# Kernel optimization log

Measured on AMD Instinct MI355X. Metric: run time of the kernel, lower is better.

## Reference

```python
import jax, jax.numpy as jnp
import numpy as np
from math import sqrt

B, N, D = 8, 4096, 512

def rotary(x, phases):
    # x: [B,N,D], phases: [B,N,D/2]
    c, s = jnp.cos(phases), jnp.sin(phases)
    a, b = jnp.split(x, 2, axis=-1)
    return jnp.concatenate([a * c - b * s, a * s + b * c], axis=-1)

def setup_inputs() -> dict:
    key = jax.random.key(0)
    ks = jax.random.split(key, 8)
    phi = jax.random.normal(ks[0], (B, N, D), dtype=jnp.float32)
    coords = jax.random.normal(ks[1], (B, N, 3), dtype=jnp.float32)
    weights = jax.random.uniform(ks[2], (B, N), dtype=jnp.float32)
    std = 1.0 / sqrt(D)
    Wq = jax.random.normal(ks[3], (D, D), dtype=jnp.float32) * std
    Wk = jax.random.normal(ks[4], (D, D), dtype=jnp.float32) * std
    Wv = jax.random.normal(ks[5], (D, D), dtype=jnp.float32) * std
    bq = jnp.zeros((D,), jnp.float32)
    bk = jnp.zeros((D,), jnp.float32)
    bv = jnp.zeros((D,), jnp.float32)
    # mode_lift weight, std = 1/kernel_scale with kernel_scale=1.0
    Wrot = jax.random.normal(ks[6], (D // 2, 3), dtype=jnp.float32)
    return {"phi": phi, "coords": coords, "weights": weights,
            "Wq": Wq, "bq": bq, "Wk": Wk, "bk": bk, "Wv": Wv, "bv": bv,
            "Wrot": Wrot}

def reference(phi, coords, weights, Wq, bq, Wk, bk, Wv, bv, Wrot):
    d = phi.shape[-1]
    q = phi @ Wq.T + bq
    k = phi @ Wk.T + bk
    v = phi @ Wv.T + bv
    # _normalize: scale query by 1/sqrt(d); attach quadrature weights to value
    q = q * (1.0 / sqrt(d))
    v = weights[..., None] * v
    # rotary positional encoding on q and k
    phases = jnp.einsum('bnc,dc->bnd', coords, Wrot)  # [B,N,D/2]
    q = rotary(q, phases)
    k = rotary(k, phases)
    # linear attention: q @ (k^T @ v), O(N*d^2)
    kv = jnp.einsum('bnd,bne->bde', k, v)   # [B,D,D]
    return jnp.einsum('bnd,bde->bne', q, kv)  # [B,N,D]
```

## Files before the change

kernel.cpp:

```cpp
#include <hip/hip_runtime.h>


typedef _Float16 f16x8 __attribute__((ext_vector_type(8)));
typedef _Float16 f16x4 __attribute__((ext_vector_type(4)));
typedef float f32x4 __attribute__((ext_vector_type(4)));

__device__ __forceinline__ void gl_lds16(const void* g, void* l) {
    __builtin_amdgcn_global_load_lds(
        (const __attribute__((address_space(1))) void*)g,
        (__attribute__((address_space(3))) void*)l, 16, 0, 0);
}

__device__ __forceinline__ void stage2(const _Float16* gA, size_t sA,
                                       const _Float16* gB, size_t sB,
                                       _Float16* As, _Float16* Bs,
                                       int ca, int srow, int sseg) {
    gl_lds16(&gA[(size_t)(ca * 16 + srow) * sA + sseg], &As[ca * 512]);
    gl_lds16(&gA[(size_t)(ca * 16 + 16 + srow) * sA + sseg], &As[(ca + 1) * 512]);
    gl_lds16(&gB[(size_t)(ca * 16 + srow) * sB + sseg], &Bs[ca * 512]);
    gl_lds16(&gB[(size_t)(ca * 16 + 16 + srow) * sB + sseg], &Bs[(ca + 1) * 512]);
}

__device__ __forceinline__ void mfma_step(const _Float16* As, const _Float16* Bs,
                                          int wm, int wn, int l16, int qs,
                                          f32x4 acc[4][4]) {
    f16x8 af[4], bf[4];
    #pragma unroll
    for (int mi = 0; mi < 4; mi++)
        af[mi] = *(const f16x8*)&As[(wm + mi * 16 + l16) * 32 + qs * 8];
    #pragma unroll
    for (int ni = 0; ni < 4; ni++)
        bf[ni] = *(const f16x8*)&Bs[(wn + ni * 16 + l16) * 32 + qs * 8];
    #pragma unroll
    for (int mi = 0; mi < 4; mi++)
        #pragma unroll
        for (int ni = 0; ni < 4; ni++)
            acc[mi][ni] = __builtin_amdgcn_mfma_f32_16x16x32_f16(
                af[mi], bf[ni], acc[mi][ni], 0, 0, 0);
}

#define PIPE_LOOP3(gA, sA, gB, sB)                                            \
    stage2(gA, sA, gB, sB, Asr[0], Bsr[0], ca, srow, sseg);                   \
    stage2(gA + 32, sA, gB + 32, sB, Asr[1], Bsr[1], ca, srow, sseg);         \
    _Pragma("unroll")                                                         \
    for (int t = 0; t < 16; t++) {                                            \
        asm volatile("s_waitcnt lgkmcnt(0)" ::: "memory");                    \
        __builtin_amdgcn_sched_barrier(0);                                    \
        if (t < 15) { asm volatile("s_waitcnt vmcnt(4)" ::: "memory"); }      \
        else        { asm volatile("s_waitcnt vmcnt(0)" ::: "memory"); }      \
        __builtin_amdgcn_s_barrier();                                         \
        asm volatile("" ::: "memory");                                        \
        __builtin_amdgcn_sched_barrier(0);                                    \
        if (t + 2 < 16)                                                       \
            stage2(gA + (size_t)(t + 2) * 32, sA,                             \
                   gB + (size_t)(t + 2) * 32, sB,                             \
                   Asr[(t + 2) % 3], Bsr[(t + 2) % 3], ca, srow, sseg);       \
        __builtin_amdgcn_s_setprio(1);                                        \
        mfma_step(Asr[t % 3], Bsr[t % 3], wm, wn, l16, qs, acc);              \
        __builtin_amdgcn_s_setprio(0);                                        \
    }

#define RING_PTRS(smem)                                                       \
    _Float16* Asr[3] = {(_Float16*)(smem), (_Float16*)(smem + 16384),         \
                        (_Float16*)(smem + 32768)};                           \
    _Float16* Bsr[3] = {(_Float16*)(smem + 8192), (_Float16*)(smem + 24576),  \
                        (_Float16*)(smem + 40960)};

__global__ __launch_bounds__(256) void convert_phi(const float* __restrict__ phi,
                                                   _Float16* __restrict__ phi_h) {
    int i = (blockIdx.x * 256 + threadIdx.x) * 4;
    float4 v = *(const float4*)(phi + i);
    f16x4 o = {(_Float16)v.x, (_Float16)v.y, (_Float16)v.z, (_Float16)v.w};
    *(f16x4*)(phi_h + i) = o;
}

__global__ __launch_bounds__(256) void pack_w(
    const float* __restrict__ Wq, const float* __restrict__ Wk,
    const float* __restrict__ Wv, const float* __restrict__ bq,
    const float* __restrict__ bk, const float* __restrict__ bv,
    _Float16* __restrict__ wcat, float* __restrict__ bcat) {
    int j = blockIdx.x;
    int reg = j >> 9, jr = j & 511;
    const float* W; const float* bias;
    if (reg == 0)      { W = Wq; bias = bq; }
    else if (reg == 1) { W = Wk; bias = bk; }
    else               { W = Wv; bias = bv; }
    int d = (reg < 2) ? ((jr & 1) ? (jr >> 1) + 256 : (jr >> 1)) : jr;
    for (int i = threadIdx.x; i < 512; i += 256)
        wcat[j * 512 + i] = (_Float16)W[d * 512 + i];
    if (threadIdx.x == 0) bcat[j] = bias[d];
}

__global__ __launch_bounds__(256) void qkv_kernel(
    const _Float16* __restrict__ phi_h, const _Float16* __restrict__ wcat,
    const float* __restrict__ bcat, const float* __restrict__ coords,
    const float* __restrict__ weights, const float* __restrict__ Wrot,
    _Float16* __restrict__ qr, _Float16* __restrict__ krT,
    _Float16* __restrict__ vwT) {
    __shared__ __align__(16) char smem[49152];
    RING_PTRS(smem)
    _Float16* Ts = (_Float16*)smem;

    const int tid = threadIdx.x;
    const int lane = tid & 63, wave = tid >> 6;
    const int quad = lane >> 4, l16 = lane & 15;
    const int qs = quad ^ ((l16 >> 1) & 3);
    const int wm = (wave >> 1) * 64, wn = (wave & 1) * 64;
    const int flat = blockIdx.x + blockIdx.y * 12;
    const int swz = (flat & 7) * 384 + (flat >> 3);
    const int c0 = (swz % 12) * 128;
    const int m0 = (swz / 12) * 128;
    const int ca = wave * 2;
    const int srow = lane >> 2;
    const int sseg = (((lane & 3) ^ ((lane >> 3) & 3)) * 8);

    const _Float16* gA = phi_h + (size_t)m0 * 512;
    const _Float16* gB = wcat + (size_t)c0 * 512;

    f32x4 acc[4][4] = {};

    PIPE_LOOP3(gA, 512, gB, 512)

    __syncthreads();

    const int region = c0 >> 9;
    const float qscale = 0.04419417382415922f;

    float bias[4], w0[4], w1[4], w2[4];
    #pragma unroll
    for (int ni = 0; ni < 4; ni++) {
        int gc = c0 + wn + ni * 16 + l16;
        bias[ni] = bcat[gc];
        if (region < 2) {
            int jp = (gc & 511) >> 1;
            w0[ni] = Wrot[jp * 3];
            w1[ni] = Wrot[jp * 3 + 1];
            w2[ni] = Wrot[jp * 3 + 2];
        }
    }

    if (region == 0) {
        #pragma unroll
        for (int mi = 0; mi < 4; mi++)
            #pragma unroll
            for (int r = 0; r < 4; r++) {
                int row = wm + mi * 16 + quad * 4 + r;
                int gm = m0 + row;
                float x = coords[gm * 3], y = coords[gm * 3 + 1], z = coords[gm * 3 + 2];
                #pragma unroll
                for (int ni = 0; ni < 4; ni++) {
                    float val = (acc[mi][ni][r] + bias[ni]) * qscale;
                    float part = __shfl_xor(val, 1);
                    float ph = x * w0[ni] + y * w1[ni] + z * w2[ni];
                    float sv, cv; __sincosf(ph, &sv, &cv);
                    float res = (l16 & 1) ? (part * sv + val * cv)
                                          : (val * cv - part * sv);
                    Ts[row * 136 + wn + ni * 16 + l16] = (_Float16)res;
                }
            }
        __syncthreads();
        for (int i = tid; i < 2048; i += 256) {
            int row = i >> 4, cv = (i & 15) * 8;
            *(f16x8*)&qr[(m0 + row) * 512 + c0 + cv] = *(f16x8*)&Ts[row * 136 + cv];
        }
    } else {
        #pragma unroll
        for (int mi = 0; mi < 4; mi++)
            #pragma unroll
            for (int r = 0; r < 4; r++) {
                int row = wm + mi * 16 + quad * 4 + r;
                int gm = m0 + row;
                if (region == 1) {
                    float x = coords[gm * 3], y = coords[gm * 3 + 1], z = coords[gm * 3 + 2];
                    #pragma unroll
                    for (int ni = 0; ni < 4; ni++) {
                        float val = acc[mi][ni][r] + bias[ni];
                        float part = __shfl_xor(val, 1);
                        float ph = x * w0[ni] + y * w1[ni] + z * w2[ni];
                        float sv, cv; __sincosf(ph, &sv, &cv);
                        float res = (l16 & 1) ? (part * sv + val * cv)
                                              : (val * cv - part * sv);
                        Ts[(wn + ni * 16 + l16) * 136 + row] = (_Float16)res;
                    }
                } else {
                    float wgt = weights[gm];
                    #pragma unroll
                    for (int ni = 0; ni < 4; ni++) {
                        float val = (acc[mi][ni][r] + bias[ni]) * wgt;
                        Ts[(wn + ni * 16 + l16) * 136 + row] = (_Float16)val;
                    }
                }
            }
        __syncthreads();
        _Float16* dst = (region == 1) ? krT : vwT;
        const int b = m0 >> 12, n0 = m0 & 4095, cb = c0 & 511;
        for (int i = tid; i < 2048; i += 256) {
            int col = i >> 4, rv = (i & 15) * 8;
            *(f16x8*)&dst[((size_t)b * 512 + cb + col) * 4096 + n0 + rv] =
                *(f16x8*)&Ts[col * 136 + rv];
        }
    }
}

__global__ __launch_bounds__(256) void kv_kernel(
    const _Float16* __restrict__ vwT, const _Float16* __restrict__ krT,
    _Float16* __restrict__ kvp) {
    __shared__ __align__(16) char smem[49152];
    RING_PTRS(smem)
    const int tid = threadIdx.x, lane = tid & 63, wave = tid >> 6;
    const int quad = lane >> 4, l16 = lane & 15;
    const int qs = quad ^ ((l16 >> 1) & 3);
    const int wm = (wave >> 1) * 64, wn = (wave & 1) * 64;
    const int flat = blockIdx.x + blockIdx.y * 4 + blockIdx.z * 16;
    const int swz = (flat & 7) * 128 + (flat >> 3);
    const int d0 = (swz & 3) * 128, e0 = ((swz >> 2) & 3) * 128;
    const int zz = swz >> 4;
    const int b = zz >> 3, split = zz & 7;
    const int ca = wave * 2;
    const int srow = lane >> 2;
    const int sseg = (((lane & 3) ^ ((lane >> 3) & 3)) * 8);
    const size_t base = (size_t)b * 512 * 4096;
    const int kbeg = split * 512;
    const _Float16* gA = vwT + base + (size_t)e0 * 4096 + kbeg;
    const _Float16* gB = krT + base + (size_t)d0 * 4096 + kbeg;
    f32x4 acc[4][4] = {};

    PIPE_LOOP3(gA, 4096, gB, 4096)

    _Float16* dst = kvp + ((size_t)split * 8 + b) * 262144;
    #pragma unroll
    for (int mi = 0; mi < 4; mi++)
        #pragma unroll
        for (int ni = 0; ni < 4; ni++)
            #pragma unroll
            for (int r = 0; r < 4; r++) {
                int e = e0 + wm + mi * 16 + quad * 4 + r;
                int d = d0 + wn + ni * 16 + l16;
                dst[e * 512 + d] = (_Float16)acc[mi][ni][r];
            }
}

__global__ __launch_bounds__(256) void reduce_kv(const _Float16* __restrict__ kvp,
                                                 _Float16* __restrict__ kvT) {
    int i = (blockIdx.x * 256 + threadIdx.x) * 8;
    float s[8] = {};
    #pragma unroll
    for (int sp = 0; sp < 8; sp++) {
        f16x8 v = *(const f16x8*)(kvp + (size_t)sp * 2097152 + i);
        #pragma unroll
        for (int j = 0; j < 8; j++) s[j] += (float)v[j];
    }
    f16x8 o;
    #pragma unroll
    for (int j = 0; j < 8; j++) o[j] = (_Float16)s[j];
    *(f16x8*)(kvT + i) = o;
}

__global__ __launch_bounds__(256) void out_kernel(
    const _Float16* __restrict__ qr, const _Float16* __restrict__ kvT,
    float* __restrict__ out) {
    __shared__ __align__(16) char smem[49152];
    RING_PTRS(smem)
    const int tid = threadIdx.x, lane = tid & 63, wave = tid >> 6;
    const int quad = lane >> 4, l16 = lane & 15;
    const int qs = quad ^ ((l16 >> 1) & 3);
    const int wm = (wave >> 1) * 64, wn = (wave & 1) * 64;
    const int flat = blockIdx.x + blockIdx.y * 4;
    const int swz = (flat & 7) * 128 + (flat >> 3);
    const int e0 = (swz & 3) * 128, m0 = (swz >> 2) * 128;
    const int b = m0 >> 12;
    const int ca = wave * 2;
    const int srow = lane >> 2;
    const int sseg = (((lane & 3) ^ ((lane >> 3) & 3)) * 8);
    const _Float16* gA = qr + (size_t)m0 * 512;
    const _Float16* gB = kvT + (size_t)b * 262144 + (size_t)e0 * 512;
    f32x4 acc[4][4] = {};

    PIPE_LOOP3(gA, 512, gB, 512)

    #pragma unroll
    for (int mi = 0; mi < 4; mi++)
        #pragma unroll
        for (int ni = 0; ni < 4; ni++)
            #pragma unroll
            for (int r = 0; r < 4; r++) {
                int gm = m0 + wm + mi * 16 + quad * 4 + r;
                int e = e0 + wn + ni * 16 + l16;
                out[(size_t)gm * 512 + e] = acc[mi][ni][r];
            }
}

extern "C" void kernel_launch(void* const* d_in, const int* in_sizes, int n_in,
                              void* d_out, int out_size, void* d_ws, size_t ws_size,
                              hipStream_t stream) {
    const float* phi     = (const float*)d_in[0];
    const float* coords  = (const float*)d_in[1];
    const float* weights = (const float*)d_in[2];
    const float* Wq      = (const float*)d_in[3];
    const float* bq      = (const float*)d_in[4];
    const float* Wk      = (const float*)d_in[5];
    const float* bk      = (const float*)d_in[6];
    const float* Wv      = (const float*)d_in[7];
    const float* bv      = (const float*)d_in[8];
    const float* Wrot    = (const float*)d_in[9];
    float* out = (float*)d_out;

    char* ws = (char*)d_ws;
    _Float16* phi_h = (_Float16*)(ws);
    _Float16* kvp   = (_Float16*)(ws);
    _Float16* wcat  = (_Float16*)(ws + 33554432);
    float*    bcat  = (float*)   (ws + 35127296);
    _Float16* qr    = (_Float16*)(ws + 35133440);
    _Float16* krT   = (_Float16*)(ws + 68687872);
    _Float16* vwT   = (_Float16*)(ws + 102242304);
    _Float16* kvT   = (_Float16*)(ws + 135796736);

    convert_phi<<<16384, 256, 0, stream>>>(phi, phi_h);
    pack_w<<<1536, 256, 0, stream>>>(Wq, Wk, Wv, bq, bk, bv, wcat, bcat);
    qkv_kernel<<<dim3(12, 256), 256, 0, stream>>>(phi_h, wcat, bcat, coords,
                                                  weights, Wrot, qr, krT, vwT);
    kv_kernel<<<dim3(4, 4, 64), 256, 0, stream>>>(vwT, krT, kvp);
    reduce_kv<<<1024, 256, 0, stream>>>(kvp, kvT);
    out_kernel<<<dim3(4, 256), 256, 0, stream>>>(qr, kvT, out);
}
```

Before: 275.1 us.

## Switch kv and out GEMMs from triple-buffered ring to double-buffered pipeline

```diff
diff --git a/kernel.cpp b/kernel.cpp
--- a/kernel.cpp
+++ b/kernel.cpp
@@ -38,6 +38,38 @@
             acc[mi][ni] = __builtin_amdgcn_mfma_f32_16x16x32_f16(
                 af[mi], bf[ni], acc[mi][ni], 0, 0, 0);
 }
+
+#define PHASE2(BUFA, BUFB, VM)                                                \
+    asm volatile("s_waitcnt vmcnt(" #VM ")" ::: "memory");                    \
+    __builtin_amdgcn_s_barrier();                                             \
+    asm volatile("" ::: "memory");                                            \
+    __builtin_amdgcn_sched_barrier(0);                                        \
+    __builtin_amdgcn_s_setprio(1);                                            \
+    mfma_step(BUFA, BUFB, wm, wn, l16, qs, acc);                              \
+    __builtin_amdgcn_s_setprio(0);                                            \
+    asm volatile("s_waitcnt lgkmcnt(0)" ::: "memory");                        \
+    __builtin_amdgcn_sched_barrier(0);                                        \
+    __builtin_amdgcn_s_barrier();                                             \
+    asm volatile("" ::: "memory");
+
+#define PIPE_LOOP2(gA, sA, gB, sB)                                            \
+    stage2(gA, sA, gB, sB, As0, Bs0, ca, srow, sseg);                         \
+    stage2(gA + 32, sA, gB + 32, sB, As1, Bs1, ca, srow, sseg);               \
+    _Pragma("unroll")                                                         \
+    for (int p = 0; p < 8; p++) {                                             \
+        const int t0 = 2 * p;                                                 \
+        PHASE2(As0, Bs0, 4)                                                   \
+        if (t0 + 2 < 16)                                                      \
+            stage2(gA + (size_t)(t0 + 2) * 32, sA,                            \
+                   gB + (size_t)(t0 + 2) * 32, sB,                            \
+                   As0, Bs0, ca, srow, sseg);                                 \
+        if (p < 7) { PHASE2(As1, Bs1, 4) }                                    \
+        else       { PHASE2(As1, Bs1, 0) }                                    \
+        if (t0 + 3 < 16)                                                      \
+            stage2(gA + (size_t)(t0 + 3) * 32, sA,                            \
+                   gB + (size_t)(t0 + 3) * 32, sB,                            \
+                   As1, Bs1, ca, srow, sseg);                                 \
+    }
 
 #define PIPE_LOOP3(gA, sA, gB, sB)                                            \
     stage2(gA, sA, gB, sB, Asr[0], Bsr[0], ca, srow, sseg);                   \
@@ -205,8 +237,11 @@
 __global__ __launch_bounds__(256) void kv_kernel(
     const _Float16* __restrict__ vwT, const _Float16* __restrict__ krT,
     _Float16* __restrict__ kvp) {
-    __shared__ __align__(16) char smem[49152];
-    RING_PTRS(smem)
+    __shared__ __align__(16) char smem[32768];
+    _Float16* As0 = (_Float16*)smem;
+    _Float16* Bs0 = (_Float16*)(smem + 8192);
+    _Float16* As1 = (_Float16*)(smem + 16384);
+    _Float16* Bs1 = (_Float16*)(smem + 24576);
     const int tid = threadIdx.x, lane = tid & 63, wave = tid >> 6;
     const int quad = lane >> 4, l16 = lane & 15;
     const int qs = quad ^ ((l16 >> 1) & 3);
@@ -225,7 +260,7 @@
     const _Float16* gB = krT + base + (size_t)d0 * 4096 + kbeg;
     f32x4 acc[4][4] = {};
 
-    PIPE_LOOP3(gA, 4096, gB, 4096)
+    PIPE_LOOP2(gA, 4096, gB, 4096)
 
     _Float16* dst = kvp + ((size_t)split * 8 + b) * 262144;
     #pragma unroll
@@ -259,8 +294,11 @@
 __global__ __launch_bounds__(256) void out_kernel(
     const _Float16* __restrict__ qr, const _Float16* __restrict__ kvT,
     float* __restrict__ out) {
-    __shared__ __align__(16) char smem[49152];
-    RING_PTRS(smem)
+    __shared__ __align__(16) char smem[32768];
+    _Float16* As0 = (_Float16*)smem;
+    _Float16* Bs0 = (_Float16*)(smem + 8192);
+    _Float16* As1 = (_Float16*)(smem + 16384);
+    _Float16* Bs1 = (_Float16*)(smem + 24576);
     const int tid = threadIdx.x, lane = tid & 63, wave = tid >> 6;
     const int quad = lane >> 4, l16 = lane & 15;
     const int qs = quad ^ ((l16 >> 1) & 3);
@@ -276,7 +314,7 @@
     const _Float16* gB = kvT + (size_t)b * 262144 + (size_t)e0 * 512;
     f32x4 acc[4][4] = {};
 
-    PIPE_LOOP3(gA, 512, gB, 512)
+    PIPE_LOOP2(gA, 512, gB, 512)
 
     #pragma unroll
     for (int mi = 0; mi < 4; mi++)
```

Result: no change. 277.5 us (+0.9%).
